# Optimization experiments

Hardware: AMD Instinct MI355X
Metric: run time of the kernel (lower is better)

Reference implementation:

```python
import jax, jax.numpy as jnp
import numpy as np

N_NODES = 100000
N_EDGES = 1600000
N_GRAPHS = 512
HIDDEN = 128
N_CLASSES = 10


def setup_inputs() -> dict:
    key = jax.random.key(0)
    ks = jax.random.split(key, 12)
    edge_index = jax.random.randint(ks[0], (2, N_EDGES), 0, N_NODES, dtype=jnp.int32)
    batch = jnp.sort(jax.random.randint(ks[1], (N_NODES,), 0, N_GRAPHS, dtype=jnp.int32))
    def lin(k, fi, fo):
        return jax.random.normal(k, (fi, fo), jnp.float32) * (1.0 / np.sqrt(fi))
    return {
        "edge_index": edge_index,
        "batch": batch,
        "W0": lin(ks[2], 1, HIDDEN),
        "b0": jax.random.normal(ks[3], (HIDDEN,), jnp.float32) * 0.01,
        "W1": lin(ks[4], HIDDEN, HIDDEN),
        "b1": jax.random.normal(ks[5], (HIDDEN,), jnp.float32) * 0.01,
        "W2": lin(ks[6], HIDDEN, HIDDEN),
        "b2": jax.random.normal(ks[7], (HIDDEN,), jnp.float32) * 0.01,
        "Wp": lin(ks[8], HIDDEN, N_CLASSES),
        "bp": jax.random.normal(ks[9], (N_CLASSES,), jnp.float32) * 0.01,
    }


def _gcn_setup(edge_index, n_nodes):
    # add self-loops (PyG GCNConv default) and compute symmetric normalization
    loop = jnp.arange(n_nodes, dtype=edge_index.dtype)
    src = jnp.concatenate([edge_index[0], loop])  # [E+N]
    dst = jnp.concatenate([edge_index[1], loop])
    deg = jax.ops.segment_sum(jnp.ones_like(src, dtype=jnp.float32), dst,
                              num_segments=n_nodes)
    dinv = jnp.where(deg > 0, jax.lax.rsqrt(deg), 0.0)
    norm = dinv[src] * dinv[dst]  # [E+N]
    return src, dst, norm


def _gcn_conv(x, W, b, src, dst, norm, n_nodes):
    h = x @ W                                # [N, out]
    msg = h[src] * norm[:, None]             # gather + scale, [E+N, out]
    out = jax.ops.segment_sum(msg, dst, num_segments=n_nodes)
    return out + b


def reference(edge_index, batch, W0, b0, W1, b1, W2, b2, Wp, bp):
    n = batch.shape[0]
    src, dst, norm = _gcn_setup(edge_index, n)
    x = jnp.ones((n, 1), jnp.float32)  # forward() hardcodes ones as features
    for W, b in ((W0, b0), (W1, b1), (W2, b2)):
        x = jax.nn.relu(_gcn_conv(x, W, b, src, dst, norm, n))
        # dropout_p = 0.0 -> identity
    # scatter_mean pooling over graphs
    s = jax.ops.segment_sum(x, batch, num_segments=N_GRAPHS)
    cnt = jax.ops.segment_sum(jnp.ones((n,), jnp.float32), batch,
                              num_segments=N_GRAPHS)
    pooled = s / jnp.maximum(cnt, 1.0)[:, None]
    logits = pooled @ Wp + bp
    return jax.nn.log_softmax(logits, axis=1)
```

## Files before the change

### kernel.cpp

```cpp
#include <hip/hip_runtime.h>

#define HID 128
#define NG 512
#define NC 10
#define BSH 9
#define BSZ (1 << BSH)
#define TILE 4096
#define NOEDGE 0xFFFFFFFFu

typedef unsigned int u32;
typedef unsigned short u16;
typedef __attribute__((ext_vector_type(8))) short short8;
typedef __attribute__((ext_vector_type(4))) float f32x4;

static __device__ __forceinline__ int gtid() {
    return blockIdx.x * blockDim.x + threadIdx.x;
}

static __device__ __forceinline__ u16 f2bf(float f) {
    u32 u = __float_as_uint(f);
    u32 r = u + 0x7fffu + ((u >> 16) & 1u);
    return (u16)(r >> 16);
}
static __device__ __forceinline__ float bf2f(u32 s) {
    return __uint_as_float(s << 16);
}
static __device__ __forceinline__ void bf8_unpack(uint4 u, float* f) {
    f[0] = bf2f(u.x & 0xffffu); f[1] = bf2f(u.x >> 16);
    f[2] = bf2f(u.y & 0xffffu); f[3] = bf2f(u.y >> 16);
    f[4] = bf2f(u.z & 0xffffu); f[5] = bf2f(u.z >> 16);
    f[6] = bf2f(u.w & 0xffffu); f[7] = bf2f(u.w >> 16);
}

__global__ __launch_bounds__(256) void k_bhist(const int* __restrict__ dst,
                                               int* __restrict__ bcnt, int E, int NB) {
    __shared__ int cnt[256];
    int t = threadIdx.x;
    int e0 = blockIdx.x * TILE;
    for (int i = t; i < NB; i += 256) cnt[i] = 0;
    __syncthreads();
#pragma unroll
    for (int k = 0; k < 16; ++k) {
        int e = e0 + k * 256 + t;
        if (e < E) atomicAdd(&cnt[dst[e] >> BSH], 1);
    }
    __syncthreads();
    for (int i = t; i < NB; i += 256)
        if (cnt[i] > 0) atomicAdd(&bcnt[i], cnt[i]);
}

__global__ __launch_bounds__(256) void k_bscan(const int* __restrict__ bcnt,
                                               int* __restrict__ bbase,
                                               int* __restrict__ bcur, int NB, int E) {
    __shared__ int s[256];
    int t = threadIdx.x;
    int own = (t < NB) ? bcnt[t] : 0;
    s[t] = own;
    __syncthreads();
    for (int off = 1; off < 256; off <<= 1) {
        int v = (t >= off) ? s[t - off] : 0;
        __syncthreads();
        s[t] += v;
        __syncthreads();
    }
    if (t < NB) {
        int b = s[t] - own;
        bbase[t] = b;
        bcur[t] = b;
    }
    if (t == 0) bbase[NB] = E;
}

__global__ __launch_bounds__(256) void k_part1(const int* __restrict__ src,
                                               const int* __restrict__ dst,
                                               int* __restrict__ bcur,
                                               u32* __restrict__ tmp, int E, int NB) {
    __shared__ int cnt[256];
    __shared__ int base[256];
    int t = threadIdx.x;
    int e0 = blockIdx.x * TILE;
    for (int i = t; i < NB; i += 256) cnt[i] = 0;
    __syncthreads();
    u32 p_[16];
    int b_[16];
#pragma unroll
    for (int k = 0; k < 16; ++k) {
        int e = e0 + k * 256 + t;
        if (e < E) {
            int d = dst[e];
            p_[k] = ((u32)src[e] << BSH) | (u32)(d & (BSZ - 1));
            b_[k] = d >> BSH;
            atomicAdd(&cnt[b_[k]], 1);
        } else {
            b_[k] = -1;
        }
    }
    __syncthreads();
    for (int i = t; i < NB; i += 256) {
        if (cnt[i] > 0) base[i] = atomicAdd(&bcur[i], cnt[i]);
        cnt[i] = 0;
    }
    __syncthreads();
#pragma unroll
    for (int k = 0; k < 16; ++k) {
        if (b_[k] >= 0) {
            int pos = base[b_[k]] + atomicAdd(&cnt[b_[k]], 1);
            tmp[pos] = p_[k];
        }
    }
}

__global__ __launch_bounds__(512) void k_part2(const int* __restrict__ bbase,
                                               const u32* __restrict__ tmp,
                                               u32* __restrict__ packed,
                                               int* __restrict__ rowptr,
                                               float* __restrict__ dinv,
                                               int N, int NB) {
    __shared__ int cnt[BSZ];
    __shared__ int scn[BSZ];
    __shared__ int cur[BSZ];
    int b = blockIdx.x;
    int v0 = b << BSH;
    int nv = N - v0; if (nv > BSZ) nv = BSZ;
    int t = threadIdx.x;
    int e0 = bbase[b], e1 = bbase[b + 1];

    cnt[t] = 0;
    __syncthreads();
    for (int e = e0 + t; e < e1; e += 512)
        atomicAdd(&cnt[tmp[e] & (BSZ - 1)], 1);
    __syncthreads();
    int own = cnt[t];
    scn[t] = own;
    __syncthreads();
    for (int off = 1; off < BSZ; off <<= 1) {
        int v = (t >= off) ? scn[t - off] : 0;
        __syncthreads();
        scn[t] += v;
        __syncthreads();
    }
    int start = e0 + scn[t] - own;
    cur[t] = start;
    if (t < nv) {
        rowptr[v0 + t] = start;
        dinv[v0 + t] = rsqrtf(1.0f + (float)own);
    }
    if (b == NB - 1 && t == 0) rowptr[N] = e1;
    __syncthreads();
    for (int e = e0 + t; e < e1; e += 512) {
        u32 p = tmp[e];
        int pos = atomicAdd(&cur[p & (BSZ - 1)], 1);
        packed[pos] = p >> BSH;
    }
}

__global__ __launch_bounds__(128) void k_sort(const float* __restrict__ W0,
                                              const float* __restrict__ b0,
                                              float* __restrict__ ts,
                                              int* __restrict__ sidx) {
    __shared__ float t[HID];
    __shared__ int ix[HID];
    int i = threadIdx.x;
    float w = W0[i];
    t[i] = (w != 0.0f) ? (-b0[i] / w) : 3.0e38f;
    ix[i] = i;
    __syncthreads();
    for (int ph = 0; ph < HID; ++ph) {
        int j = 2 * i + (ph & 1);
        if (j + 1 < HID) {
            if (t[j] > t[j + 1]) {
                float tv = t[j]; t[j] = t[j + 1]; t[j + 1] = tv;
                int iv = ix[j]; ix[j] = ix[j + 1]; ix[j + 1] = iv;
            }
        }
        __syncthreads();
    }
    ts[i] = t[i];
    sidx[i] = ix[i];
}

__global__ __launch_bounds__(128) void k_tab(const float* __restrict__ W0,
                                             const float* __restrict__ b0,
                                             const float* __restrict__ W1,
                                             const int* __restrict__ sidx,
                                             float* __restrict__ A,
                                             float* __restrict__ Bt) {
    __shared__ float w0s[HID], b0s[HID];
    __shared__ int ds[HID];
    int r = blockIdx.x;
    int j = threadIdx.x;
    ds[j] = sidx[j];
    w0s[j] = W0[ds[j]];
    b0s[j] = b0[ds[j]];
    __syncthreads();
    float a = 0.0f, b = 0.0f;
    for (int p = 0; p < HID; ++p) {
        int d = ds[p];
        float w0 = w0s[p];
        bool act = (w0 != 0.0f) ? ((w0 > 0.0f) ? (p < r) : (p >= r)) : (b0s[p] > 0.0f);
        if (act) {
            float w1 = W1[d * HID + j];
            a = fmaf(w0, w1, a);
            b = fmaf(b0s[p], w1, b);
        }
    }
    A[r * HID + j] = a;
    Bt[r * HID + j] = b;
}

__global__ __launch_bounds__(256) void k_l01(const int* __restrict__ rowptr,
                                             const u32* __restrict__ packed,
                                             const float* __restrict__ dinv,
                                             const float* __restrict__ ts,
                                             const float* __restrict__ A,
                                             const float* __restrict__ Bt,
                                             u16* __restrict__ q, int N) {
    __shared__ float tls[HID];
    if (threadIdx.x < HID) tls[threadIdx.x] = ts[threadIdx.x];
    __syncthreads();
    int lane = threadIdx.x & 31;
    int v = (blockIdx.x * 256 + threadIdx.x) >> 5;
    if (v >= N) return;
    int r0 = rowptr[v], r1 = rowptr[v + 1];
    float s = 0.0f;
    for (int j = r0 + lane; j < r1; j += 32) s += dinv[packed[j]];
#pragma unroll
    for (int off = 16; off > 0; off >>= 1) s += __shfl_xor(s, off, 32);
    float di = dinv[v];
    s = di * (di + s);
    int lo = 0, hi = HID;
    while (lo < hi) {
        int mid = (lo + hi) >> 1;
        if (tls[mid] < s) lo = mid + 1; else hi = mid;
    }
    int r = lo;
    int d0 = lane * 4;
    float4 av = *(const float4*)&A[r * HID + d0];
    float4 bv = *(const float4*)&Bt[r * HID + d0];
    float q0 = di * fmaf(av.x, s, bv.x);
    float q1 = di * fmaf(av.y, s, bv.y);
    float q2 = di * fmaf(av.z, s, bv.z);
    float q3 = di * fmaf(av.w, s, bv.w);
    uint2 o;
    o.x = (u32)f2bf(q0) | ((u32)f2bf(q1) << 16);
    o.y = (u32)f2bf(q2) | ((u32)f2bf(q3) << 16);
    *(uint2*)&q[(size_t)v * HID + d0] = o;
}

__global__ __launch_bounds__(256) void k_wt(const float* __restrict__ W,
                                            u16* __restrict__ Wt) {
    int t = gtid();
    if (t >= 2048) return;
    int n = t >> 4;
    int j = t & 15;
    int js = j ^ (n & 7);
    u32 w0 = (u32)f2bf(W[(j * 8 + 0) * HID + n]) | ((u32)f2bf(W[(j * 8 + 1) * HID + n]) << 16);
    u32 w1 = (u32)f2bf(W[(j * 8 + 2) * HID + n]) | ((u32)f2bf(W[(j * 8 + 3) * HID + n]) << 16);
    u32 w2 = (u32)f2bf(W[(j * 8 + 4) * HID + n]) | ((u32)f2bf(W[(j * 8 + 5) * HID + n]) << 16);
    u32 w3 = (u32)f2bf(W[(j * 8 + 6) * HID + n]) | ((u32)f2bf(W[(j * 8 + 7) * HID + n]) << 16);
    uint4 o = make_uint4(w0, w1, w2, w3);
    *(uint4*)&Wt[(size_t)n * HID + js * 8] = o;
}

__global__ __launch_bounds__(256) void k_gemm(const u16* __restrict__ x,
                                              const u16* __restrict__ Wt,
                                              const float* __restrict__ dinv,
                                              u16* __restrict__ q, int nrows) {
    __shared__ u16 Wl[HID * HID];
    int tid = threadIdx.x;
    for (int i = tid; i < 2048; i += 256)
        *(uint4*)&Wl[i * 8] = *(const uint4*)&Wt[i * 8];

    int w = tid >> 6;
    int l = tid & 63;
    int R0 = blockIdx.x * 64 + w * 16;
    int arow = R0 + (l & 15);
    int koff = (l >> 4) * 8;

    short8 a[4];
#pragma unroll
    for (int kb = 0; kb < 4; ++kb) {
        if (arow < nrows)
            a[kb] = *(const short8*)&x[(size_t)arow * HID + kb * 32 + koff];
        else
            a[kb] = (short8)0;
    }
    __syncthreads();

    int colbase = l & 15;
    int rowq = (l >> 4) * 4;
    float dv[4];
#pragma unroll
    for (int i = 0; i < 4; ++i) {
        int orow = R0 + rowq + i;
        dv[i] = (orow < nrows) ? dinv[orow] : 0.0f;
    }
#pragma unroll
    for (int cb = 0; cb < 8; ++cb) {
        f32x4 acc = {0.0f, 0.0f, 0.0f, 0.0f};
        int wrow = cb * 16 + (l & 15);
#pragma unroll
        for (int kb = 0; kb < 4; ++kb) {
            int j = (kb * 4 + (l >> 4)) ^ (wrow & 7);
            short8 b = *(const short8*)&Wl[wrow * HID + j * 8];
            acc = __builtin_amdgcn_mfma_f32_16x16x32_bf16(a[kb], b, acc, 0, 0, 0);
        }
#pragma unroll
        for (int i = 0; i < 4; ++i) {
            int orow = R0 + rowq + i;
            if (orow < nrows)
                q[(size_t)orow * HID + cb * 16 + colbase] = f2bf(acc[i] * dv[i]);
        }
    }
}

__global__ __launch_bounds__(256) void k_aggr(const u32* __restrict__ packed,
                                              const int* __restrict__ rowptr,
                                              const u16* __restrict__ q,
                                              const float* __restrict__ dinv,
                                              const float* __restrict__ b,
                                              u16* __restrict__ y, int N) {
    int lane = threadIdx.x & 63;
    int v = (blockIdx.x * 256 + threadIdx.x) >> 6;
    if (v >= N) return;
    int r0 = rowptr[v], r1 = rowptr[v + 1];
    int q4 = lane >> 4;
    int d8 = (lane & 15) * 8;

    float acc[8];
    if (q4 == 0) {
        uint4 qv = *(const uint4*)&q[(size_t)v * HID + d8];
        bf8_unpack(qv, acc);
    } else {
#pragma unroll
        for (int j = 0; j < 8; ++j) acc[j] = 0.0f;
    }

    for (int base = r0; base < r1; base += 64) {
        int idx = base + lane;
        u32 e = (idx < r1) ? packed[idx] : NOEDGE;
        int m = r1 - base; if (m > 64) m = 64;
        int iters = (m + 3) >> 2;
        int k = 0;
        for (; k + 2 <= iters; k += 2) {
            u32 s0 = __shfl(e, 4 * k + q4, 64);
            u32 s1 = __shfl(e, 4 * k + 4 + q4, 64);
            uint4 h0 = make_uint4(0, 0, 0, 0);
            uint4 h1 = make_uint4(0, 0, 0, 0);
            if (s0 != NOEDGE) h0 = *(const uint4*)&q[(size_t)s0 * HID + d8];
            if (s1 != NOEDGE) h1 = *(const uint4*)&q[(size_t)s1 * HID + d8];
            float f0[8], f1[8];
            bf8_unpack(h0, f0);
            bf8_unpack(h1, f1);
#pragma unroll
            for (int j = 0; j < 8; ++j) acc[j] += f0[j] + f1[j];
        }
        if (k < iters) {
            u32 s0 = __shfl(e, 4 * k + q4, 64);
            if (s0 != NOEDGE) {
                uint4 h0 = *(const uint4*)&q[(size_t)s0 * HID + d8];
                float f0[8];
                bf8_unpack(h0, f0);
#pragma unroll
                for (int j = 0; j < 8; ++j) acc[j] += f0[j];
            }
        }
    }
#pragma unroll
    for (int j = 0; j < 8; ++j) {
        acc[j] += __shfl_xor(acc[j], 16, 64);
        acc[j] += __shfl_xor(acc[j], 32, 64);
    }

    if (q4 == 0) {
        float dv = dinv[v];
        float4 b0 = *(const float4*)&b[d8];
        float4 b1 = *(const float4*)&b[d8 + 4];
        float o[8];
        o[0] = fmaxf(fmaf(acc[0], dv, b0.x), 0.0f);
        o[1] = fmaxf(fmaf(acc[1], dv, b0.y), 0.0f);
        o[2] = fmaxf(fmaf(acc[2], dv, b0.z), 0.0f);
        o[3] = fmaxf(fmaf(acc[3], dv, b0.w), 0.0f);
        o[4] = fmaxf(fmaf(acc[4], dv, b1.x), 0.0f);
        o[5] = fmaxf(fmaf(acc[5], dv, b1.y), 0.0f);
        o[6] = fmaxf(fmaf(acc[6], dv, b1.z), 0.0f);
        o[7] = fmaxf(fmaf(acc[7], dv, b1.w), 0.0f);
        uint4 u;
        u.x = (u32)f2bf(o[0]) | ((u32)f2bf(o[1]) << 16);
        u.y = (u32)f2bf(o[2]) | ((u32)f2bf(o[3]) << 16);
        u.z = (u32)f2bf(o[4]) | ((u32)f2bf(o[5]) << 16);
        u.w = (u32)f2bf(o[6]) | ((u32)f2bf(o[7]) << 16);
        *(uint4*)&y[(size_t)v * HID + d8] = u;
    }
}

__global__ __launch_bounds__(256) void k_pool(const u16* __restrict__ x,
                                              const int* __restrict__ batch,
                                              float* __restrict__ pooled,
                                              float* __restrict__ cntg, int N) {
    const int K = 32;
    int grp = threadIdx.x >> 4;
    int lane16 = threadIdx.x & 15;
    int d8 = lane16 * 8;
    int chunk = blockIdx.x * 16 + grp;
    int v0 = chunk * K;
    if (v0 >= N) return;
    int vend = v0 + K; if (vend > N) vend = N;
    int g = batch[v0];
    float acc[8] = {0, 0, 0, 0, 0, 0, 0, 0};
    float c = 0.0f;
    for (int v = v0; v < vend; ++v) {
        int gv = batch[v];
        if (gv != g) {
#pragma unroll
            for (int j = 0; j < 8; ++j) atomicAdd(&pooled[g * HID + d8 + j], acc[j]);
            if (lane16 == 0) atomicAdd(&cntg[g], c);
#pragma unroll
            for (int j = 0; j < 8; ++j) acc[j] = 0.0f;
            c = 0.0f; g = gv;
        }
        uint4 u = *(const uint4*)&x[(size_t)v * HID + d8];
        float f[8];
        bf8_unpack(u, f);
#pragma unroll
        for (int j = 0; j < 8; ++j) acc[j] += f[j];
        c += 1.0f;
    }
#pragma unroll
    for (int j = 0; j < 8; ++j) atomicAdd(&pooled[g * HID + d8 + j], acc[j]);
    if (lane16 == 0) atomicAdd(&cntg[g], c);
}

__global__ void k_head(const float* __restrict__ pooled, const float* __restrict__ cnt,
                       const float* __restrict__ Wp, const float* __restrict__ bp,
                       float* __restrict__ out) {
    int g = gtid();
    if (g >= NG) return;
    float inv = 1.0f / fmaxf(cnt[g], 1.0f);
    float l[NC];
#pragma unroll
    for (int c = 0; c < NC; ++c) l[c] = bp[c];
    for (int d = 0; d < HID; ++d) {
        float pv = pooled[g * HID + d] * inv;
#pragma unroll
        for (int c = 0; c < NC; ++c) l[c] = fmaf(pv, Wp[d * NC + c], l[c]);
    }
    float m = l[0];
#pragma unroll
    for (int c = 1; c < NC; ++c) m = fmaxf(m, l[c]);
    float s = 0.0f;
#pragma unroll
    for (int c = 0; c < NC; ++c) s += expf(l[c] - m);
    float ls = logf(s) + m;
#pragma unroll
    for (int c = 0; c < NC; ++c) out[g * NC + c] = l[c] - ls;
}

extern "C" void kernel_launch(void* const* d_in, const int* in_sizes, int n_in,
                              void* d_out, int out_size, void* d_ws, size_t ws_size,
                              hipStream_t stream) {
    const int* ei    = (const int*)d_in[0];
    int E            = in_sizes[0] / 2;
    const int* src   = ei;
    const int* dstp  = ei + E;
    const int* batch = (const int*)d_in[1];
    int N            = in_sizes[1];
    const float* W0  = (const float*)d_in[2];
    const float* b0  = (const float*)d_in[3];
    const float* W1  = (const float*)d_in[4];
    const float* b1  = (const float*)d_in[5];
    const float* W2  = (const float*)d_in[6];
    const float* b2  = (const float*)d_in[7];
    const float* Wp  = (const float*)d_in[8];
    const float* bp  = (const float*)d_in[9];
    float* out       = (float*)d_out;

    u16*  xA     = (u16*)d_ws;
    u16*  xB     = xA + (size_t)N * HID;
    u32*  packed = (u32*)(xB + (size_t)N * HID);
    u32*  tmp    = packed + E;
    u16*  Wt2    = (u16*)(tmp + E);
    float* A     = (float*)(Wt2 + HID * HID);
    float* Bt    = A + 129 * HID;
    float* ts    = Bt + 129 * HID;
    int*  sidx   = (int*)(ts + HID);
    int*  rowptr = sidx + HID;
    int*  bcnt   = rowptr + N + 1;
    int*  bbase  = bcnt + 256;
    int*  bcur   = bbase + 257;
    float* dinv  = (float*)(bcur + 256);
    float* pooled= dinv + N;
    float* cntg  = pooled + NG * HID;

    auto cdiv = [](int a, int b) { return (a + b - 1) / b; };
    int NB = cdiv(N, BSZ);

    hipMemsetAsync(bcnt, 0, 256 * sizeof(int), stream);
    hipMemsetAsync(pooled, 0, (NG * HID + NG) * sizeof(float), stream);

    k_bhist<<<cdiv(E, TILE), 256, 0, stream>>>(dstp, bcnt, E, NB);
    k_bscan<<<1, 256, 0, stream>>>(bcnt, bbase, bcur, NB, E);
    k_part1<<<cdiv(E, TILE), 256, 0, stream>>>(src, dstp, bcur, tmp, E, NB);
    k_part2<<<NB, 512, 0, stream>>>(bbase, tmp, packed, rowptr, dinv, N, NB);

    k_sort<<<1, 128, 0, stream>>>(W0, b0, ts, sidx);
    k_tab<<<129, 128, 0, stream>>>(W0, b0, W1, sidx, A, Bt);
    k_wt<<<8, 256, 0, stream>>>(W2, Wt2);

    k_l01<<<cdiv(N, 8), 256, 0, stream>>>(rowptr, packed, dinv, ts, A, Bt, xB, N);

    k_aggr<<<cdiv(N, 4), 256, 0, stream>>>(packed, rowptr, xB, dinv, b1, xA, N);

    k_gemm<<<cdiv(N, 64), 256, 0, stream>>>(xA, Wt2, dinv, xB, N);
    k_aggr<<<cdiv(N, 4), 256, 0, stream>>>(packed, rowptr, xB, dinv, b2, xA, N);

    k_pool<<<cdiv(cdiv(N, 32), 16), 256, 0, stream>>>(xA, batch, pooled, cntg, N);
    k_head<<<2, 256, 0, stream>>>(pooled, cntg, Wp, bp, out);
}
```

Measured before the change: 326.0 us.

## Aggregate layer-1 from per-node scalars and LDS lookup tables instead of gathering rows

Layer-1 messages no longer materialise a 128-wide bf16 row per node. Each node instead stores a compact (scale, row index, dinv) record, and the aggregation kernel rebuilds each neighbour's contribution from bf16 A/B tables held in shared memory. This replaces the gather of a 256-byte row per edge with an 8-byte gather plus LDS reads. It also swaps the odd-even transposition sort for a bitonic sort, narrows the layer-2 aggregation from 64 to 32 lanes per node, and merges the two memsets. The costs are extra bf16 rounding in the tables, a large LDS footprint limiting occupancy, and a fixed grid of 256 blocks.

```diff
diff --git a/kernel.cpp b/kernel.cpp
--- a/kernel.cpp
+++ b/kernel.cpp
@@ -165,15 +165,19 @@
     t[i] = (w != 0.0f) ? (-b0[i] / w) : 3.0e38f;
     ix[i] = i;
     __syncthreads();
-    for (int ph = 0; ph < HID; ++ph) {
-        int j = 2 * i + (ph & 1);
-        if (j + 1 < HID) {
-            if (t[j] > t[j + 1]) {
-                float tv = t[j]; t[j] = t[j + 1]; t[j + 1] = tv;
-                int iv = ix[j]; ix[j] = ix[j + 1]; ix[j + 1] = iv;
+    for (int k = 2; k <= HID; k <<= 1) {
+        for (int j = k >> 1; j > 0; j >>= 1) {
+            int p = i ^ j;
+            if (p > i) {
+                bool up = ((i & k) == 0);
+                float ti = t[i], tp = t[p];
+                if ((ti > tp) == up) {
+                    t[i] = tp; t[p] = ti;
+                    int a = ix[i]; ix[i] = ix[p]; ix[p] = a;
+                }
             }
-        }
-        __syncthreads();
+            __syncthreads();
+        }
     }
     ts[i] = t[i];
     sidx[i] = ix[i];
@@ -183,8 +187,8 @@
                                              const float* __restrict__ b0,
                                              const float* __restrict__ W1,
                                              const int* __restrict__ sidx,
-                                             float* __restrict__ A,
-                                             float* __restrict__ Bt) {
+                                             u16* __restrict__ Ab,
+                                             u16* __restrict__ Bb) {
     __shared__ float w0s[HID], b0s[HID];
     __shared__ int ds[HID];
     int r = blockIdx.x;
@@ -204,17 +208,15 @@
             b = fmaf(b0s[p], w1, b);
         }
     }
-    A[r * HID + j] = a;
-    Bt[r * HID + j] = b;
-}
-
-__global__ __launch_bounds__(256) void k_l01(const int* __restrict__ rowptr,
-                                             const u32* __restrict__ packed,
-                                             const float* __restrict__ dinv,
-                                             const float* __restrict__ ts,
-                                             const float* __restrict__ A,
-                                             const float* __restrict__ Bt,
-                                             u16* __restrict__ q, int N) {
+    Ab[r * HID + j] = f2bf(a);
+    Bb[r * HID + j] = f2bf(b);
+}
+
+__global__ __launch_bounds__(256) void k_SP(const int* __restrict__ rowptr,
+                                            const u32* __restrict__ packed,
+                                            const float* __restrict__ dinv,
+                                            const float* __restrict__ ts,
+                                            uint2* __restrict__ SP, int N) {
     __shared__ float tls[HID];
     if (threadIdx.x < HID) tls[threadIdx.x] = ts[threadIdx.x];
     __syncthreads();
@@ -227,24 +229,105 @@
 #pragma unroll
     for (int off = 16; off > 0; off >>= 1) s += __shfl_xor(s, off, 32);
     float di = dinv[v];
-    s = di * (di + s);
+    float S = di * (di + s);
     int lo = 0, hi = HID;
     while (lo < hi) {
         int mid = (lo + hi) >> 1;
-        if (tls[mid] < s) lo = mid + 1; else hi = mid;
-    }
-    int r = lo;
-    int d0 = lane * 4;
-    float4 av = *(const float4*)&A[r * HID + d0];
-    float4 bv = *(const float4*)&Bt[r * HID + d0];
-    float q0 = di * fmaf(av.x, s, bv.x);
-    float q1 = di * fmaf(av.y, s, bv.y);
-    float q2 = di * fmaf(av.z, s, bv.z);
-    float q3 = di * fmaf(av.w, s, bv.w);
-    uint2 o;
-    o.x = (u32)f2bf(q0) | ((u32)f2bf(q1) << 16);
-    o.y = (u32)f2bf(q2) | ((u32)f2bf(q3) << 16);
-    *(uint2*)&q[(size_t)v * HID + d0] = o;
+        if (tls[mid] < S) lo = mid + 1; else hi = mid;
+    }
+    if (lane == 0)
+        SP[v] = make_uint2(__float_as_uint(di * S), ((u32)lo << 16) | (u32)f2bf(di));
+}
+
+__global__ __launch_bounds__(512) void k_aggrT(const u32* __restrict__ packed,
+                                               const int* __restrict__ rowptr,
+                                               const uint2* __restrict__ SP,
+                                               const float* __restrict__ dinv,
+                                               const u16* __restrict__ Ab,
+                                               const u16* __restrict__ Bb,
+                                               const float* __restrict__ b1,
+                                               u16* __restrict__ y, int N, int chunk) {
+    __shared__ __align__(16) u16 As[129 * HID];
+    __shared__ __align__(16) u16 Bs[129 * HID];
+    int tid = threadIdx.x;
+    for (int u = tid; u < 129 * 16; u += 512) {
+        ((uint4*)As)[u] = ((const uint4*)Ab)[u];
+        ((uint4*)Bs)[u] = ((const uint4*)Bb)[u];
+    }
+    __syncthreads();
+
+    int g = tid >> 5;
+    int lane = tid & 31;
+    int d4 = lane * 4;
+    int v0 = blockIdx.x * chunk;
+    int vend = v0 + chunk; if (vend > N) vend = N;
+
+    for (int v = v0 + g; v < vend; v += 16) {
+        int r0 = rowptr[v], r1 = rowptr[v + 1];
+        float acc[4] = {0.0f, 0.0f, 0.0f, 0.0f};
+        {
+            uint2 sp = SP[v];
+            float a = __uint_as_float(sp.x);
+            int r = sp.y >> 16;
+            float c = bf2f(sp.y & 0xffffu);
+            uint2 Aq = ((const uint2*)As)[r * 32 + lane];
+            uint2 Bq = ((const uint2*)Bs)[r * 32 + lane];
+            acc[0] += bf2f(Aq.x & 0xffffu) * a + bf2f(Bq.x & 0xffffu) * c;
+            acc[1] += bf2f(Aq.x >> 16)     * a + bf2f(Bq.x >> 16)     * c;
+            acc[2] += bf2f(Aq.y & 0xffffu) * a + bf2f(Bq.y & 0xffffu) * c;
+            acc[3] += bf2f(Aq.y >> 16)     * a + bf2f(Bq.y >> 16)     * c;
+        }
+        for (int base = r0; base < r1; base += 32) {
+            int idx = base + lane;
+            float a_l = 0.0f; u32 m_l = 0;
+            if (idx < r1) {
+                uint2 sp = SP[packed[idx]];
+                a_l = __uint_as_float(sp.x);
+                m_l = sp.y;
+            }
+            int m = r1 - base; if (m > 32) m = 32;
+            int k = 0;
+            for (; k + 2 <= m; k += 2) {
+                float a0 = __shfl(a_l, k, 32);     u32 m0 = __shfl((int)m_l, k, 32);
+                float a1 = __shfl(a_l, k + 1, 32); u32 m1 = __shfl((int)m_l, k + 1, 32);
+                int  rA = m0 >> 16, rB = m1 >> 16;
+                float c0 = bf2f(m0 & 0xffffu), c1 = bf2f(m1 & 0xffffu);
+                uint2 Aq0 = ((const uint2*)As)[rA * 32 + lane];
+                uint2 Bq0 = ((const uint2*)Bs)[rA * 32 + lane];
+                uint2 Aq1 = ((const uint2*)As)[rB * 32 + lane];
+                uint2 Bq1 = ((const uint2*)Bs)[rB * 32 + lane];
+                acc[0] += bf2f(Aq0.x & 0xffffu) * a0 + bf2f(Bq0.x & 0xffffu) * c0
+                        + bf2f(Aq1.x & 0xffffu) * a1 + bf2f(Bq1.x & 0xffffu) * c1;
+                acc[1] += bf2f(Aq0.x >> 16)     * a0 + bf2f(Bq0.x >> 16)     * c0
+                        + bf2f(Aq1.x >> 16)     * a1 + bf2f(Bq1.x >> 16)     * c1;
+                acc[2] += bf2f(Aq0.y & 0xffffu) * a0 + bf2f(Bq0.y & 0xffffu) * c0
+                        + bf2f(Aq1.y & 0xffffu) * a1 + bf2f(Bq1.y & 0xffffu) * c1;
+                acc[3] += bf2f(Aq0.y >> 16)     * a0 + bf2f(Bq0.y >> 16)     * c0
+                        + bf2f(Aq1.y >> 16)     * a1 + bf2f(Bq1.y >> 16)     * c1;
+            }
+            if (k < m) {
+                float a0 = __shfl(a_l, k, 32); u32 m0 = __shfl((int)m_l, k, 32);
+                int rA = m0 >> 16;
+                float c0 = bf2f(m0 & 0xffffu);
+                uint2 Aq0 = ((const uint2*)As)[rA * 32 + lane];
+                uint2 Bq0 = ((const uint2*)Bs)[rA * 32 + lane];
+                acc[0] += bf2f(Aq0.x & 0xffffu) * a0 + bf2f(Bq0.x & 0xffffu) * c0;
+                acc[1] += bf2f(Aq0.x >> 16)     * a0 + bf2f(Bq0.x >> 16)     * c0;
+                acc[2] += bf2f(Aq0.y & 0xffffu) * a0 + bf2f(Bq0.y & 0xffffu) * c0;
+                acc[3] += bf2f(Aq0.y >> 16)     * a0 + bf2f(Bq0.y >> 16)     * c0;
+            }
+        }
+        float dv = dinv[v];
+        float4 bv = *(const float4*)&b1[d4];
+        float o0 = fmaxf(fmaf(acc[0], dv, bv.x), 0.0f);
+        float o1 = fmaxf(fmaf(acc[1], dv, bv.y), 0.0f);
+        float o2 = fmaxf(fmaf(acc[2], dv, bv.z), 0.0f);
+        float o3 = fmaxf(fmaf(acc[3], dv, bv.w), 0.0f);
+        uint2 u;
+        u.x = (u32)f2bf(o0) | ((u32)f2bf(o1) << 16);
+        u.y = (u32)f2bf(o2) | ((u32)f2bf(o3) << 16);
+        *(uint2*)&y[(size_t)v * HID + d4] = u;
+    }
 }
 
 __global__ __launch_bounds__(256) void k_wt(const float* __restrict__ W,
@@ -320,15 +403,15 @@
                                               const float* __restrict__ dinv,
                                               const float* __restrict__ b,
                                               u16* __restrict__ y, int N) {
-    int lane = threadIdx.x & 63;
-    int v = (blockIdx.x * 256 + threadIdx.x) >> 6;
+    int lane = threadIdx.x & 31;
+    int v = (blockIdx.x * 256 + threadIdx.x) >> 5;
     if (v >= N) return;
     int r0 = rowptr[v], r1 = rowptr[v + 1];
-    int q4 = lane >> 4;
+    int half = lane >> 4;
     int d8 = (lane & 15) * 8;
 
     float acc[8];
-    if (q4 == 0) {
+    if (half == 0) {
         uint4 qv = *(const uint4*)&q[(size_t)v * HID + d8];
         bf8_unpack(qv, acc);
     } else {
@@ -336,15 +419,15 @@
         for (int j = 0; j < 8; ++j) acc[j] = 0.0f;
     }
 
-    for (int base = r0; base < r1; base += 64) {
+    for (int base = r0; base < r1; base += 32) {
         int idx = base + lane;
         u32 e = (idx < r1) ? packed[idx] : NOEDGE;
-        int m = r1 - base; if (m > 64) m = 64;
-        int iters = (m + 3) >> 2;
+        int m = r1 - base; if (m > 32) m = 32;
+        int iters = (m + 1) >> 1;
         int k = 0;
         for (; k + 2 <= iters; k += 2) {
-            u32 s0 = __shfl(e, 4 * k + q4, 64);
-            u32 s1 = __shfl(e, 4 * k + 4 + q4, 64);
+            u32 s0 = __shfl(e, 2 * k + half, 32);
+            u32 s1 = __shfl(e, 2 * k + 2 + half, 32);
             uint4 h0 = make_uint4(0, 0, 0, 0);
             uint4 h1 = make_uint4(0, 0, 0, 0);
             if (s0 != NOEDGE) h0 = *(const uint4*)&q[(size_t)s0 * HID + d8];
@@ -356,7 +439,7 @@
             for (int j = 0; j < 8; ++j) acc[j] += f0[j] + f1[j];
         }
         if (k < iters) {
-            u32 s0 = __shfl(e, 4 * k + q4, 64);
+            u32 s0 = __shfl(e, 2 * k + half, 32);
             if (s0 != NOEDGE) {
                 uint4 h0 = *(const uint4*)&q[(size_t)s0 * HID + d8];
                 float f0[8];
@@ -367,12 +450,9 @@
         }
     }
 #pragma unroll
-    for (int j = 0; j < 8; ++j) {
-        acc[j] += __shfl_xor(acc[j], 16, 64);
-        acc[j] += __shfl_xor(acc[j], 32, 64);
-    }
-
-    if (q4 == 0) {
+    for (int j = 0; j < 8; ++j) acc[j] += __shfl_xor(acc[j], 16, 32);
+
+    if (half == 0) {
         float dv = dinv[v];
         float4 b0 = *(const float4*)&b[d8];
         float4 b1 = *(const float4*)&b[d8 + 4];
@@ -479,24 +559,25 @@
     u16*  xB     = xA + (size_t)N * HID;
     u32*  packed = (u32*)(xB + (size_t)N * HID);
     u32*  tmp    = packed + E;
-    u16*  Wt2    = (u16*)(tmp + E);
-    float* A     = (float*)(Wt2 + HID * HID);
-    float* Bt    = A + 129 * HID;
-    float* ts    = Bt + 129 * HID;
+    uint2* SP    = (uint2*)(tmp + E);
+    u16*  Wt2    = (u16*)(SP + N);
+    u16*  Ab     = Wt2 + HID * HID;
+    u16*  Bb     = Ab + 129 * HID;
+    float* ts    = (float*)(Bb + 129 * HID);
     int*  sidx   = (int*)(ts + HID);
     int*  rowptr = sidx + HID;
-    int*  bcnt   = rowptr + N + 1;
-    int*  bbase  = bcnt + 256;
+    int*  bbase  = rowptr + N + 1;
     int*  bcur   = bbase + 257;
     float* dinv  = (float*)(bcur + 256);
     float* pooled= dinv + N;
     float* cntg  = pooled + NG * HID;
+    int*  bcnt   = (int*)(cntg + NG);
 
     auto cdiv = [](int a, int b) { return (a + b - 1) / b; };
     int NB = cdiv(N, BSZ);
-
-    hipMemsetAsync(bcnt, 0, 256 * sizeof(int), stream);
-    hipMemsetAsync(pooled, 0, (NG * HID + NG) * sizeof(float), stream);
+    int chunkT = cdiv(N, 256);
+
+    hipMemsetAsync(pooled, 0, (NG * HID + NG + 256) * sizeof(float), stream);
 
     k_bhist<<<cdiv(E, TILE), 256, 0, stream>>>(dstp, bcnt, E, NB);
     k_bscan<<<1, 256, 0, stream>>>(bcnt, bbase, bcur, NB, E);
@@ -504,15 +585,14 @@
     k_part2<<<NB, 512, 0, stream>>>(bbase, tmp, packed, rowptr, dinv, N, NB);
 
     k_sort<<<1, 128, 0, stream>>>(W0, b0, ts, sidx);
-    k_tab<<<129, 128, 0, stream>>>(W0, b0, W1, sidx, A, Bt);
+    k_tab<<<129, 128, 0, stream>>>(W0, b0, W1, sidx, Ab, Bb);
     k_wt<<<8, 256, 0, stream>>>(W2, Wt2);
-
-    k_l01<<<cdiv(N, 8), 256, 0, stream>>>(rowptr, packed, dinv, ts, A, Bt, xB, N);
-
-    k_aggr<<<cdiv(N, 4), 256, 0, stream>>>(packed, rowptr, xB, dinv, b1, xA, N);
+    k_SP<<<cdiv(N, 8), 256, 0, stream>>>(rowptr, packed, dinv, ts, SP, N);
+
+    k_aggrT<<<256, 512, 0, stream>>>(packed, rowptr, SP, dinv, Ab, Bb, b1, xA, N, chunkT);
 
     k_gemm<<<cdiv(N, 64), 256, 0, stream>>>(xA, Wt2, dinv, xB, N);
-    k_aggr<<<cdiv(N, 4), 256, 0, stream>>>(packed, rowptr, xB, dinv, b2, xA, N);
+    k_aggr<<<cdiv(N, 8), 256, 0, stream>>>(packed, rowptr, xB, dinv, b2, xA, N);
 
     k_pool<<<cdiv(cdiv(N, 32), 16), 256, 0, stream>>>(xA, batch, pooled, cntg, N);
     k_head<<<2, 256, 0, stream>>>(pooled, cntg, Wp, bp, out);
```

After: 311.8 us. -4.3%, faster.
